# Optimization experiments

Hardware: AMD Instinct MI355X
Metric: run time of the kernel (lower is better)

The kernel has to match this reference:

```python
import jax, jax.numpy as jnp
import numpy as np

BATCH, D_INNER, DT_RANK, N = 256, 5120, 160, 16

def _softplus_thresh(z, threshold=20.0):
    # softplus(z) with beta=1; linear above threshold (matches ttnn.softplus(parameter1=1, parameter2=20))
    return jnp.where(z > threshold, z, jax.nn.softplus(z))

def setup_inputs() -> dict:
    key = jax.random.key(0)
    ks = jax.random.split(key, 9)
    s = lambda d: 1.0 / np.sqrt(d)
    return {
        "x": jax.random.normal(ks[0], (1, 1, BATCH, D_INNER), jnp.float32),
        "h": jax.random.normal(ks[1], (BATCH, D_INNER, N), jnp.float32) * 0.1,
        "W_delta": jax.random.normal(ks[2], (D_INNER, DT_RANK), jnp.float32) * s(D_INNER),
        "W_dt": jax.random.normal(ks[3], (DT_RANK, D_INNER), jnp.float32) * s(DT_RANK),
        "b_dt": jax.random.normal(ks[4], (D_INNER,), jnp.float32) * 0.1,
        "A_log": jax.random.uniform(ks[5], (D_INNER, N), jnp.float32, 0.0, 1.5),
        "W_B": jax.random.normal(ks[6], (D_INNER, N), jnp.float32) * s(D_INNER),
        "W_C": jax.random.normal(ks[7], (D_INNER, N), jnp.float32) * s(D_INNER),
        "D": jax.random.normal(ks[8], (D_INNER,), jnp.float32),
    }

def reference(x, h, W_delta, W_dt, b_dt, A_log, W_B, W_C, D):
    # x: (1,1,B,d_inner) single decode step; h: (B,d_inner,n) SSM state
    xb = x.reshape(BATCH, D_INNER)                           # (B, d)
    # delta = softplus(x @ W_delta @ W_dt + b_dt)           -> (B, d)
    dt = _softplus_thresh((xb @ W_delta) @ W_dt + b_dt)
    A = -jnp.exp(A_log)                                      # (d, n)
    abar = jnp.exp(dt[:, :, None] * A[None, :, :])           # (B, d, n)
    Bp = xb @ W_B                                            # (B, n)
    # bbar * x: delta * B * x, broadcast over state dim
    bx = (dt * xb)[:, :, None] * Bp[:, None, :]              # (B, d, n)
    h_new = abar * h + bx                                    # (B, d, n) new hidden state
    C = xb @ W_C                                             # (B, n)
    y = jnp.einsum("bdn,bn->bd", h_new, C) + xb * D          # readout + skip (D)
    return y.reshape(1, 1, BATCH, D_INNER)
```

## Files before the change

kernel.cpp:

```cpp
#include <hip/hip_runtime.h>
#include <math.h>

#define BATCH 256
#define DIN   5120
#define RANK  160
#define NS    16
#define NCAT  192
#define NSPLIT 40

__global__ __launch_bounds__(256) void k1a_gemm(
    const float* __restrict__ x, const float* __restrict__ Wd,
    const float* __restrict__ WB, const float* __restrict__ WC,
    float* __restrict__ psum)
{
    __shared__ float xT[32][64];
    __shared__ float Wt[32][64];
    const int t  = threadIdx.x;
    const int m0 = blockIdx.x * 64;
    const int n0 = blockIdx.y * 64;
    const int z  = blockIdx.z;
    const int k0 = z * 128;
    const int tm = (t >> 4) * 4;
    const int tn = (t & 15) * 4;

    const int lm  = t >> 2;
    const int lk  = (t & 3) * 8;
    const int ln  = t & 63;
    const int lkb = (t >> 6) * 8;

    const float* wsrc; int wstr;
    {
        const int c = n0 + ln;
        if (c < RANK)            { wsrc = Wd + c;                wstr = RANK; }
        else if (c < RANK + NS)  { wsrc = WB + (c - RANK);       wstr = NS;   }
        else                     { wsrc = WC + (c - RANK - NS);  wstr = NS;   }
    }

    float acc[4][4] = {{0.f}};

    for (int ks = 0; ks < 4; ++ks) {
        const int kb = k0 + ks * 32;
        {
            const float* src = x + (size_t)(m0 + lm) * DIN + kb + lk;
            const float4 a0 = *(const float4*)src;
            const float4 a1 = *(const float4*)(src + 4);
            xT[lk+0][lm]=a0.x; xT[lk+1][lm]=a0.y; xT[lk+2][lm]=a0.z; xT[lk+3][lm]=a0.w;
            xT[lk+4][lm]=a1.x; xT[lk+5][lm]=a1.y; xT[lk+6][lm]=a1.z; xT[lk+7][lm]=a1.w;
        }
        {
            const float* wp = wsrc + (size_t)(kb + lkb) * wstr;
            #pragma unroll
            for (int i = 0; i < 8; ++i) { Wt[lkb + i][ln] = *wp; wp += wstr; }
        }
        __syncthreads();
        #pragma unroll
        for (int k = 0; k < 32; ++k) {
            const float4 a = *(const float4*)&xT[k][tm];
            const float4 b = *(const float4*)&Wt[k][tn];
            acc[0][0] += a.x*b.x; acc[0][1] += a.x*b.y; acc[0][2] += a.x*b.z; acc[0][3] += a.x*b.w;
            acc[1][0] += a.y*b.x; acc[1][1] += a.y*b.y; acc[1][2] += a.y*b.z; acc[1][3] += a.y*b.w;
            acc[2][0] += a.z*b.x; acc[2][1] += a.z*b.y; acc[2][2] += a.z*b.z; acc[2][3] += a.z*b.w;
            acc[3][0] += a.w*b.x; acc[3][1] += a.w*b.y; acc[3][2] += a.w*b.z; acc[3][3] += a.w*b.w;
        }
        __syncthreads();
    }

    float* dst = psum + (size_t)z * (BATCH * NCAT);
    #pragma unroll
    for (int i = 0; i < 4; ++i) {
        const int gm = m0 + tm + i;
        float4 o; o.x = acc[i][0]; o.y = acc[i][1]; o.z = acc[i][2]; o.w = acc[i][3];
        *(float4*)&dst[(size_t)gm * NCAT + n0 + tn] = o;
    }
}

__global__ __launch_bounds__(256) void k1r_reduce(
    const float* __restrict__ psum, float* __restrict__ P,
    float* __restrict__ Bp, float* __restrict__ Cc)
{
    const int o = blockIdx.x * 256 + threadIdx.x;
    float s = 0.f;
    #pragma unroll 8
    for (int z = 0; z < NSPLIT; ++z) s += psum[(size_t)z * (BATCH * NCAT) + o];
    const int gm = o / NCAT;
    const int gc = o - gm * NCAT;
    if (gc < RANK)           P [gm * RANK + gc]             = s;
    else if (gc < RANK + NS) Bp[gm * NS   + gc - RANK]      = s;
    else                     Cc[gm * NS   + gc - RANK - NS] = s;
}

__device__ __forceinline__ float softplus20(float z)
{
    if (z > 20.f) return z;
    return fmaxf(z, 0.f) + log1pf(__expf(-fabsf(z)));
}

__global__ __launch_bounds__(256) void k2a_gemm(
    const float* __restrict__ P, const float* __restrict__ Wdt,
    const float* __restrict__ bdt, float* __restrict__ dtb)
{
    __shared__ float aT[32][64];
    __shared__ float Bt[32][64];
    const int t  = threadIdx.x;
    const int m0 = blockIdx.x * 64;
    const int n0 = blockIdx.y * 64;
    const int tm = (t >> 4) * 4;
    const int tn = (t & 15) * 4;

    const int lm  = t >> 2;
    const int lk  = (t & 3) * 8;
    const int ln  = t & 63;
    const int lkb = (t >> 6) * 8;

    float acc[4][4] = {{0.f}};

    for (int ks = 0; ks < 5; ++ks) {
        const int kb = ks * 32;
        {
            const float* src = P + (size_t)(m0 + lm) * RANK + kb + lk;
            const float4 a0 = *(const float4*)src;
            const float4 a1 = *(const float4*)(src + 4);
            aT[lk+0][lm]=a0.x; aT[lk+1][lm]=a0.y; aT[lk+2][lm]=a0.z; aT[lk+3][lm]=a0.w;
            aT[lk+4][lm]=a1.x; aT[lk+5][lm]=a1.y; aT[lk+6][lm]=a1.z; aT[lk+7][lm]=a1.w;
        }
        {
            const float* wp = Wdt + (size_t)(kb + lkb) * DIN + n0 + ln;
            #pragma unroll
            for (int i = 0; i < 8; ++i) { Bt[lkb + i][ln] = wp[(size_t)i * DIN]; }
        }
        __syncthreads();
        #pragma unroll
        for (int k = 0; k < 32; ++k) {
            const float4 a = *(const float4*)&aT[k][tm];
            const float4 b = *(const float4*)&Bt[k][tn];
            acc[0][0] += a.x*b.x; acc[0][1] += a.x*b.y; acc[0][2] += a.x*b.z; acc[0][3] += a.x*b.w;
            acc[1][0] += a.y*b.x; acc[1][1] += a.y*b.y; acc[1][2] += a.y*b.z; acc[1][3] += a.y*b.w;
            acc[2][0] += a.z*b.x; acc[2][1] += a.z*b.y; acc[2][2] += a.z*b.z; acc[2][3] += a.z*b.w;
            acc[3][0] += a.w*b.x; acc[3][1] += a.w*b.y; acc[3][2] += a.w*b.z; acc[3][3] += a.w*b.w;
        }
        __syncthreads();
    }

    const float4 bz = *(const float4*)&bdt[n0 + tn];
    #pragma unroll
    for (int i = 0; i < 4; ++i) {
        const int gm = m0 + tm + i;
        float4 o;
        o.x = softplus20(acc[i][0] + bz.x);
        o.y = softplus20(acc[i][1] + bz.y);
        o.z = softplus20(acc[i][2] + bz.z);
        o.w = softplus20(acc[i][3] + bz.w);
        *(float4*)&dtb[(size_t)gm * DIN + n0 + tn] = o;
    }
}

__global__ __launch_bounds__(256) void k3_ssm(
    const float* __restrict__ dtb, const float* __restrict__ x,
    const float* __restrict__ h, const float* __restrict__ A_log,
    const float* __restrict__ Bp, const float* __restrict__ Cc,
    const float* __restrict__ Dv, float* __restrict__ y)
{
    const int t    = threadIdx.x;
    const int lane = t & 63;
    const int wv   = t >> 6;
    const int b    = blockIdx.x / 20;
    const int d0   = (blockIdx.x % 20) * 256 + wv * 64;

    const int v = lane & 3;
    const int j = lane >> 2;

    const float4 B4 = *(const float4*)(Bp + b * NS + v * 4);
    const float4 C4 = *(const float4*)(Cc + b * NS + v * 4);

    float res[4];
    #pragma unroll
    for (int q = 0; q < 4; ++q) {
        const int c = d0 + q * 16 + j;
        const float dtv = dtb[(size_t)b * DIN + c];
        const float xv  = x  [(size_t)b * DIN + c];
        const float dtx = dtv * xv;
        const float4 h4 = *(const float4*)(h     + ((size_t)b * DIN + c) * NS + v * 4);
        const float4 a4 = *(const float4*)(A_log + (size_t)c * NS + v * 4);
        float s;
        s  = (exp2f(dtv * (-1.442695041f * __expf(a4.x))) * h4.x + dtx * B4.x) * C4.x;
        s += (exp2f(dtv * (-1.442695041f * __expf(a4.y))) * h4.y + dtx * B4.y) * C4.y;
        s += (exp2f(dtv * (-1.442695041f * __expf(a4.z))) * h4.z + dtx * B4.z) * C4.z;
        s += (exp2f(dtv * (-1.442695041f * __expf(a4.w))) * h4.w + dtx * B4.w) * C4.w;
        if (v == 0) s += xv * Dv[c];
        res[q] = s;
    }

    #pragma unroll
    for (int q = 0; q < 4; ++q) {
        res[q] += __shfl_xor(res[q], 1, 64);
        res[q] += __shfl_xor(res[q], 2, 64);
    }
    if (v == 0) {
        #pragma unroll
        for (int q = 0; q < 4; ++q)
            y[(size_t)b * DIN + d0 + q * 16 + j] = res[q];
    }
}

extern "C" void kernel_launch(void* const* d_in, const int* in_sizes, int n_in,
                              void* d_out, int out_size, void* d_ws, size_t ws_size,
                              hipStream_t stream)
{
    const float* x     = (const float*)d_in[0];
    const float* h     = (const float*)d_in[1];
    const float* Wd    = (const float*)d_in[2];
    const float* Wdt   = (const float*)d_in[3];
    const float* bdt   = (const float*)d_in[4];
    const float* A_log = (const float*)d_in[5];
    const float* WB    = (const float*)d_in[6];
    const float* WC    = (const float*)d_in[7];
    const float* Dv    = (const float*)d_in[8];
    float* out = (float*)d_out;

    float* psum = (float*)d_ws;
    float* P    = psum + (size_t)NSPLIT * BATCH * NCAT;
    float* Bp   = P  + BATCH * RANK;
    float* Cc   = Bp + BATCH * NS;
    float* dtb  = Cc + BATCH * NS;

    k1a_gemm  <<<dim3(4, 3, NSPLIT), 256, 0, stream>>>(x, Wd, WB, WC, psum);
    k1r_reduce<<<dim3(NCAT),         256, 0, stream>>>(psum, P, Bp, Cc);
    k2a_gemm  <<<dim3(4, 80),        256, 0, stream>>>(P, Wdt, bdt, dtb);
    k3_ssm    <<<dim3(BATCH * 20),   256, 0, stream>>>(dtb, x, h, A_log, Bp, Cc, Dv, out);
}
```

Measured before the change: 182.2 us.

## Fuse dt GEMM into SSM kernel and precompute scaled A in reduce

Merges the second projection GEMM (P @ W_dt + softplus) into the SSM update kernel. Each block computes dt for 8 batch rows by 256 channels into shared memory and then consumes it directly, which removes the dtb round trip through global memory and one launch. The reduce kernel now also precomputes -log2(e)*exp(A_log) once, so the SSM loop no longer does a per-element exp on A. The fused GEMM is a plain per-thread dot product that reads the W_dt column uncoalesced-strided over k and P through broadcast loads, with no shared-memory tiling, so it may cost more ALU and memory time than the old tiled GEMM.

```diff
diff --git a/kernel.cpp b/kernel.cpp
--- a/kernel.cpp
+++ b/kernel.cpp
@@ -7,6 +7,7 @@
 #define NS    16
 #define NCAT  192
 #define NSPLIT 40
+#define BQ    8
 
 __global__ __launch_bounds__(256) void k1a_gemm(
     const float* __restrict__ x, const float* __restrict__ Wd,
@@ -75,18 +76,24 @@
 }
 
 __global__ __launch_bounds__(256) void k1r_reduce(
-    const float* __restrict__ psum, float* __restrict__ P,
-    float* __restrict__ Bp, float* __restrict__ Cc)
-{
-    const int o = blockIdx.x * 256 + threadIdx.x;
-    float s = 0.f;
-    #pragma unroll 8
-    for (int z = 0; z < NSPLIT; ++z) s += psum[(size_t)z * (BATCH * NCAT) + o];
-    const int gm = o / NCAT;
-    const int gc = o - gm * NCAT;
-    if (gc < RANK)           P [gm * RANK + gc]             = s;
-    else if (gc < RANK + NS) Bp[gm * NS   + gc - RANK]      = s;
-    else                     Cc[gm * NS   + gc - RANK - NS] = s;
+    const float* __restrict__ psum, const float* __restrict__ A_log,
+    float* __restrict__ P, float* __restrict__ Bp, float* __restrict__ Cc,
+    float* __restrict__ A2t)
+{
+    const int g = blockIdx.x * 256 + threadIdx.x;
+    A2t[g] = -1.442695041f * __expf(A_log[g]);
+
+    if (blockIdx.x < NCAT) {
+        const int o = blockIdx.x * 256 + threadIdx.x;
+        float s = 0.f;
+        #pragma unroll 8
+        for (int z = 0; z < NSPLIT; ++z) s += psum[(size_t)z * (BATCH * NCAT) + o];
+        const int gm = o / NCAT;
+        const int gc = o - gm * NCAT;
+        if (gc < RANK)           P [gm * RANK + gc]             = s;
+        else if (gc < RANK + NS) Bp[gm * NS   + gc - RANK]      = s;
+        else                     Cc[gm * NS   + gc - RANK - NS] = s;
+    }
 }
 
 __device__ __forceinline__ float softplus20(float z)
@@ -95,110 +102,82 @@
     return fmaxf(z, 0.f) + log1pf(__expf(-fabsf(z)));
 }
 
-__global__ __launch_bounds__(256) void k2a_gemm(
+__global__ __launch_bounds__(256) void k23_ssm(
     const float* __restrict__ P, const float* __restrict__ Wdt,
-    const float* __restrict__ bdt, float* __restrict__ dtb)
-{
-    __shared__ float aT[32][64];
-    __shared__ float Bt[32][64];
-    const int t  = threadIdx.x;
-    const int m0 = blockIdx.x * 64;
-    const int n0 = blockIdx.y * 64;
-    const int tm = (t >> 4) * 4;
-    const int tn = (t & 15) * 4;
-
-    const int lm  = t >> 2;
-    const int lk  = (t & 3) * 8;
-    const int ln  = t & 63;
-    const int lkb = (t >> 6) * 8;
-
-    float acc[4][4] = {{0.f}};
-
-    for (int ks = 0; ks < 5; ++ks) {
-        const int kb = ks * 32;
-        {
-            const float* src = P + (size_t)(m0 + lm) * RANK + kb + lk;
-            const float4 a0 = *(const float4*)src;
-            const float4 a1 = *(const float4*)(src + 4);
-            aT[lk+0][lm]=a0.x; aT[lk+1][lm]=a0.y; aT[lk+2][lm]=a0.z; aT[lk+3][lm]=a0.w;
-            aT[lk+4][lm]=a1.x; aT[lk+5][lm]=a1.y; aT[lk+6][lm]=a1.z; aT[lk+7][lm]=a1.w;
-        }
-        {
-            const float* wp = Wdt + (size_t)(kb + lkb) * DIN + n0 + ln;
-            #pragma unroll
-            for (int i = 0; i < 8; ++i) { Bt[lkb + i][ln] = wp[(size_t)i * DIN]; }
-        }
-        __syncthreads();
-        #pragma unroll
-        for (int k = 0; k < 32; ++k) {
-            const float4 a = *(const float4*)&aT[k][tm];
-            const float4 b = *(const float4*)&Bt[k][tn];
-            acc[0][0] += a.x*b.x; acc[0][1] += a.x*b.y; acc[0][2] += a.x*b.z; acc[0][3] += a.x*b.w;
-            acc[1][0] += a.y*b.x; acc[1][1] += a.y*b.y; acc[1][2] += a.y*b.z; acc[1][3] += a.y*b.w;
-            acc[2][0] += a.z*b.x; acc[2][1] += a.z*b.y; acc[2][2] += a.z*b.z; acc[2][3] += a.z*b.w;
-            acc[3][0] += a.w*b.x; acc[3][1] += a.w*b.y; acc[3][2] += a.w*b.z; acc[3][3] += a.w*b.w;
-        }
-        __syncthreads();
-    }
-
-    const float4 bz = *(const float4*)&bdt[n0 + tn];
-    #pragma unroll
-    for (int i = 0; i < 4; ++i) {
-        const int gm = m0 + tm + i;
-        float4 o;
-        o.x = softplus20(acc[i][0] + bz.x);
-        o.y = softplus20(acc[i][1] + bz.y);
-        o.z = softplus20(acc[i][2] + bz.z);
-        o.w = softplus20(acc[i][3] + bz.w);
-        *(float4*)&dtb[(size_t)gm * DIN + n0 + tn] = o;
-    }
-}
-
-__global__ __launch_bounds__(256) void k3_ssm(
-    const float* __restrict__ dtb, const float* __restrict__ x,
-    const float* __restrict__ h, const float* __restrict__ A_log,
+    const float* __restrict__ bdt, const float* __restrict__ x,
+    const float* __restrict__ h, const float* __restrict__ A2t,
     const float* __restrict__ Bp, const float* __restrict__ Cc,
     const float* __restrict__ Dv, float* __restrict__ y)
 {
-    const int t    = threadIdx.x;
+    __shared__ float sdt[BQ][256];
+
+    const int t  = threadIdx.x;
+    const int ct = blockIdx.x % 20;
+    const int bg = blockIdx.x / 20;
+    const int c0 = ct * 256;
+    const int b0 = bg * BQ;
+
+    {
+        const int c = c0 + t;
+        float acc[BQ];
+        #pragma unroll
+        for (int b = 0; b < BQ; ++b) acc[b] = 0.f;
+        const float* wcol = Wdt + c;
+        const float* Pb   = P + (size_t)b0 * RANK;
+        #pragma unroll 4
+        for (int k = 0; k < RANK; ++k) {
+            const float w = wcol[(size_t)k * DIN];
+            #pragma unroll
+            for (int b = 0; b < BQ; ++b) acc[b] += Pb[b * RANK + k] * w;
+        }
+        const float bb = bdt[c];
+        #pragma unroll
+        for (int b = 0; b < BQ; ++b) sdt[b][t] = softplus20(acc[b] + bb);
+    }
+    __syncthreads();
+
     const int lane = t & 63;
     const int wv   = t >> 6;
-    const int b    = blockIdx.x / 20;
-    const int d0   = (blockIdx.x % 20) * 256 + wv * 64;
-
-    const int v = lane & 3;
-    const int j = lane >> 2;
-
-    const float4 B4 = *(const float4*)(Bp + b * NS + v * 4);
-    const float4 C4 = *(const float4*)(Cc + b * NS + v * 4);
-
-    float res[4];
+    const int v    = lane & 3;
+    const int j    = lane >> 2;
+    const int cb   = c0 + wv * 64;
+
+    float4 A2q[4];
     #pragma unroll
-    for (int q = 0; q < 4; ++q) {
-        const int c = d0 + q * 16 + j;
-        const float dtv = dtb[(size_t)b * DIN + c];
-        const float xv  = x  [(size_t)b * DIN + c];
-        const float dtx = dtv * xv;
-        const float4 h4 = *(const float4*)(h     + ((size_t)b * DIN + c) * NS + v * 4);
-        const float4 a4 = *(const float4*)(A_log + (size_t)c * NS + v * 4);
-        float s;
-        s  = (exp2f(dtv * (-1.442695041f * __expf(a4.x))) * h4.x + dtx * B4.x) * C4.x;
-        s += (exp2f(dtv * (-1.442695041f * __expf(a4.y))) * h4.y + dtx * B4.y) * C4.y;
-        s += (exp2f(dtv * (-1.442695041f * __expf(a4.z))) * h4.z + dtx * B4.z) * C4.z;
-        s += (exp2f(dtv * (-1.442695041f * __expf(a4.w))) * h4.w + dtx * B4.w) * C4.w;
-        if (v == 0) s += xv * Dv[c];
-        res[q] = s;
-    }
-
-    #pragma unroll
-    for (int q = 0; q < 4; ++q) {
-        res[q] += __shfl_xor(res[q], 1, 64);
-        res[q] += __shfl_xor(res[q], 2, 64);
-    }
-    if (v == 0) {
-        #pragma unroll
-        for (int q = 0; q < 4; ++q)
-            y[(size_t)b * DIN + d0 + q * 16 + j] = res[q];
+    for (int q = 0; q < 4; ++q)
+        A2q[q] = *(const float4*)(A2t + (size_t)(cb + q * 16 + j) * NS + v * 4);
+
+    #pragma unroll 2
+    for (int b = 0; b < BQ; ++b) {
+        const int gb = b0 + b;
+        const float4 B4 = *(const float4*)(Bp + gb * NS + v * 4);
+        const float4 C4 = *(const float4*)(Cc + gb * NS + v * 4);
+        float res[4];
+        #pragma unroll
+        for (int q = 0; q < 4; ++q) {
+            const int cq  = cb + q * 16 + j;
+            const float dtv = sdt[b][wv * 64 + q * 16 + j];
+            const float xv  = x[(size_t)gb * DIN + cq];
+            const float dtx = dtv * xv;
+            const float4 h4 = *(const float4*)(h + ((size_t)gb * DIN + cq) * NS + v * 4);
+            float s;
+            s  = (exp2f(dtv * A2q[q].x) * h4.x + dtx * B4.x) * C4.x;
+            s += (exp2f(dtv * A2q[q].y) * h4.y + dtx * B4.y) * C4.y;
+            s += (exp2f(dtv * A2q[q].z) * h4.z + dtx * B4.z) * C4.z;
+            s += (exp2f(dtv * A2q[q].w) * h4.w + dtx * B4.w) * C4.w;
+            if (v == 0) s += xv * Dv[cq];
+            res[q] = s;
+        }
+        #pragma unroll
+        for (int q = 0; q < 4; ++q) {
+            res[q] += __shfl_xor(res[q], 1, 64);
+            res[q] += __shfl_xor(res[q], 2, 64);
+        }
+        if (v == 0) {
+            #pragma unroll
+            for (int q = 0; q < 4; ++q)
+                y[(size_t)gb * DIN + cb + q * 16 + j] = res[q];
+        }
     }
 }
 
@@ -221,10 +200,9 @@
     float* P    = psum + (size_t)NSPLIT * BATCH * NCAT;
     float* Bp   = P  + BATCH * RANK;
     float* Cc   = Bp + BATCH * NS;
-    float* dtb  = Cc + BATCH * NS;
-
-    k1a_gemm  <<<dim3(4, 3, NSPLIT), 256, 0, stream>>>(x, Wd, WB, WC, psum);
-    k1r_reduce<<<dim3(NCAT),         256, 0, stream>>>(psum, P, Bp, Cc);
-    k2a_gemm  <<<dim3(4, 80),        256, 0, stream>>>(P, Wdt, bdt, dtb);
-    k3_ssm    <<<dim3(BATCH * 20),   256, 0, stream>>>(dtb, x, h, A_log, Bp, Cc, Dv, out);
-}
+    float* A2t  = Cc + BATCH * NS;
+
+    k1a_gemm  <<<dim3(4, 3, NSPLIT),   256, 0, stream>>>(x, Wd, WB, WC, psum);
+    k1r_reduce<<<dim3(320),            256, 0, stream>>>(psum, A_log, P, Bp, Cc, A2t);
+    k23_ssm   <<<dim3(20 * BATCH/BQ),  256, 0, stream>>>(P, Wdt, bdt, x, h, A2t, Bp, Cc, Dv, out);
+}
```

After: 198.1 us. 8.7% more time.

## Fuse dt GEMM with SSM update and precompute scaled A in reduce kernel

Applied to the files above, without the earlier changes.

Merges the dt projection GEMM and the SSM state-update kernel so each block computes a 64x64 tile of softplus(dt) into shared memory and consumes it directly, removing the dtb global round trip and one launch. The reduce kernel is widened to also precompute -log2(e)*exp(A_log) once, so the SSM stage no longer recomputes an exp per element per batch. The fused grid has only 320 blocks each looping over 16 batches per wave, which cuts parallelism for the memory-bound h stream and adds 16KB of shared memory per block.

```diff
diff --git a/kernel.cpp b/kernel.cpp
--- a/kernel.cpp
+++ b/kernel.cpp
@@ -75,18 +75,24 @@
 }
 
 __global__ __launch_bounds__(256) void k1r_reduce(
-    const float* __restrict__ psum, float* __restrict__ P,
-    float* __restrict__ Bp, float* __restrict__ Cc)
-{
-    const int o = blockIdx.x * 256 + threadIdx.x;
-    float s = 0.f;
-    #pragma unroll 8
-    for (int z = 0; z < NSPLIT; ++z) s += psum[(size_t)z * (BATCH * NCAT) + o];
-    const int gm = o / NCAT;
-    const int gc = o - gm * NCAT;
-    if (gc < RANK)           P [gm * RANK + gc]             = s;
-    else if (gc < RANK + NS) Bp[gm * NS   + gc - RANK]      = s;
-    else                     Cc[gm * NS   + gc - RANK - NS] = s;
+    const float* __restrict__ psum, const float* __restrict__ A_log,
+    float* __restrict__ P, float* __restrict__ Bp, float* __restrict__ Cc,
+    float* __restrict__ A2t)
+{
+    const int g = blockIdx.x * 256 + threadIdx.x;
+    A2t[g] = -1.442695041f * __expf(A_log[g]);
+
+    if (blockIdx.x < NCAT) {
+        const int o = blockIdx.x * 256 + threadIdx.x;
+        float s = 0.f;
+        #pragma unroll 8
+        for (int z = 0; z < NSPLIT; ++z) s += psum[(size_t)z * (BATCH * NCAT) + o];
+        const int gm = o / NCAT;
+        const int gc = o - gm * NCAT;
+        if (gc < RANK)           P [gm * RANK + gc]             = s;
+        else if (gc < RANK + NS) Bp[gm * NS   + gc - RANK]      = s;
+        else                     Cc[gm * NS   + gc - RANK - NS] = s;
+    }
 }
 
 __device__ __forceinline__ float softplus20(float z)
@@ -95,110 +101,116 @@
     return fmaxf(z, 0.f) + log1pf(__expf(-fabsf(z)));
 }
 
-__global__ __launch_bounds__(256) void k2a_gemm(
+__global__ __launch_bounds__(256) void k23_ssm(
     const float* __restrict__ P, const float* __restrict__ Wdt,
-    const float* __restrict__ bdt, float* __restrict__ dtb)
+    const float* __restrict__ bdt, const float* __restrict__ x,
+    const float* __restrict__ h, const float* __restrict__ A2t,
+    const float* __restrict__ Bp, const float* __restrict__ Cc,
+    const float* __restrict__ Dv, float* __restrict__ y)
 {
     __shared__ float aT[32][64];
     __shared__ float Bt[32][64];
+    __shared__ float sdt[64][64];
+
     const int t  = threadIdx.x;
-    const int m0 = blockIdx.x * 64;
-    const int n0 = blockIdx.y * 64;
-    const int tm = (t >> 4) * 4;
-    const int tn = (t & 15) * 4;
-
-    const int lm  = t >> 2;
-    const int lk  = (t & 3) * 8;
-    const int ln  = t & 63;
-    const int lkb = (t >> 6) * 8;
-
-    float acc[4][4] = {{0.f}};
-
-    for (int ks = 0; ks < 5; ++ks) {
-        const int kb = ks * 32;
-        {
-            const float* src = P + (size_t)(m0 + lm) * RANK + kb + lk;
-            const float4 a0 = *(const float4*)src;
-            const float4 a1 = *(const float4*)(src + 4);
-            aT[lk+0][lm]=a0.x; aT[lk+1][lm]=a0.y; aT[lk+2][lm]=a0.z; aT[lk+3][lm]=a0.w;
-            aT[lk+4][lm]=a1.x; aT[lk+5][lm]=a1.y; aT[lk+6][lm]=a1.z; aT[lk+7][lm]=a1.w;
-        }
-        {
-            const float* wp = Wdt + (size_t)(kb + lkb) * DIN + n0 + ln;
+    const int c0 = blockIdx.x * 64;
+    const int b0 = blockIdx.y * 64;
+
+    {
+        const int tm = (t >> 4) * 4;
+        const int tn = (t & 15) * 4;
+        const int lm  = t >> 2;
+        const int lk  = (t & 3) * 8;
+        const int ln  = t & 63;
+        const int lkb = (t >> 6) * 8;
+
+        float acc[4][4] = {{0.f}};
+
+        for (int ks = 0; ks < 5; ++ks) {
+            const int kb = ks * 32;
+            {
+                const float* src = P + (size_t)(b0 + lm) * RANK + kb + lk;
+                const float4 a0 = *(const float4*)src;
+                const float4 a1 = *(const float4*)(src + 4);
+                aT[lk+0][lm]=a0.x; aT[lk+1][lm]=a0.y; aT[lk+2][lm]=a0.z; aT[lk+3][lm]=a0.w;
+                aT[lk+4][lm]=a1.x; aT[lk+5][lm]=a1.y; aT[lk+6][lm]=a1.z; aT[lk+7][lm]=a1.w;
+            }
+            {
+                const float* wp = Wdt + (size_t)(kb + lkb) * DIN + c0 + ln;
+                #pragma unroll
+                for (int i = 0; i < 8; ++i) { Bt[lkb + i][ln] = wp[(size_t)i * DIN]; }
+            }
+            __syncthreads();
             #pragma unroll
-            for (int i = 0; i < 8; ++i) { Bt[lkb + i][ln] = wp[(size_t)i * DIN]; }
-        }
-        __syncthreads();
-        #pragma unroll
-        for (int k = 0; k < 32; ++k) {
-            const float4 a = *(const float4*)&aT[k][tm];
-            const float4 b = *(const float4*)&Bt[k][tn];
-            acc[0][0] += a.x*b.x; acc[0][1] += a.x*b.y; acc[0][2] += a.x*b.z; acc[0][3] += a.x*b.w;
-            acc[1][0] += a.y*b.x; acc[1][1] += a.y*b.y; acc[1][2] += a.y*b.z; acc[1][3] += a.y*b.w;
-            acc[2][0] += a.z*b.x; acc[2][1] += a.z*b.y; acc[2][2] += a.z*b.z; acc[2][3] += a.z*b.w;
-            acc[3][0] += a.w*b.x; acc[3][1] += a.w*b.y; acc[3][2] += a.w*b.z; acc[3][3] += a.w*b.w;
-        }
-        __syncthreads();
-    }
-
-    const float4 bz = *(const float4*)&bdt[n0 + tn];
-    #pragma unroll
-    for (int i = 0; i < 4; ++i) {
-        const int gm = m0 + tm + i;
-        float4 o;
-        o.x = softplus20(acc[i][0] + bz.x);
-        o.y = softplus20(acc[i][1] + bz.y);
-        o.z = softplus20(acc[i][2] + bz.z);
-        o.w = softplus20(acc[i][3] + bz.w);
-        *(float4*)&dtb[(size_t)gm * DIN + n0 + tn] = o;
-    }
-}
-
-__global__ __launch_bounds__(256) void k3_ssm(
-    const float* __restrict__ dtb, const float* __restrict__ x,
-    const float* __restrict__ h, const float* __restrict__ A_log,
-    const float* __restrict__ Bp, const float* __restrict__ Cc,
-    const float* __restrict__ Dv, float* __restrict__ y)
-{
-    const int t    = threadIdx.x;
+            for (int k = 0; k < 32; ++k) {
+                const float4 a = *(const float4*)&aT[k][tm];
+                const float4 b = *(const float4*)&Bt[k][tn];
+                acc[0][0] += a.x*b.x; acc[0][1] += a.x*b.y; acc[0][2] += a.x*b.z; acc[0][3] += a.x*b.w;
+                acc[1][0] += a.y*b.x; acc[1][1] += a.y*b.y; acc[1][2] += a.y*b.z; acc[1][3] += a.y*b.w;
+                acc[2][0] += a.z*b.x; acc[2][1] += a.z*b.y; acc[2][2] += a.z*b.z; acc[2][3] += a.z*b.w;
+                acc[3][0] += a.w*b.x; acc[3][1] += a.w*b.y; acc[3][2] += a.w*b.z; acc[3][3] += a.w*b.w;
+            }
+            __syncthreads();
+        }
+
+        const float4 bz = *(const float4*)&bdt[c0 + tn];
+        #pragma unroll
+        for (int i = 0; i < 4; ++i) {
+            float4 o;
+            o.x = softplus20(acc[i][0] + bz.x);
+            o.y = softplus20(acc[i][1] + bz.y);
+            o.z = softplus20(acc[i][2] + bz.z);
+            o.w = softplus20(acc[i][3] + bz.w);
+            *(float4*)&sdt[tm + i][tn] = o;
+        }
+    }
+    __syncthreads();
+
     const int lane = t & 63;
     const int wv   = t >> 6;
-    const int b    = blockIdx.x / 20;
-    const int d0   = (blockIdx.x % 20) * 256 + wv * 64;
-
-    const int v = lane & 3;
-    const int j = lane >> 2;
-
-    const float4 B4 = *(const float4*)(Bp + b * NS + v * 4);
-    const float4 C4 = *(const float4*)(Cc + b * NS + v * 4);
-
-    float res[4];
+    const int v    = lane & 3;
+    const int j    = lane >> 2;
+
+    float4 A2q[4]; float dvq[4];
     #pragma unroll
     for (int q = 0; q < 4; ++q) {
-        const int c = d0 + q * 16 + j;
-        const float dtv = dtb[(size_t)b * DIN + c];
-        const float xv  = x  [(size_t)b * DIN + c];
-        const float dtx = dtv * xv;
-        const float4 h4 = *(const float4*)(h     + ((size_t)b * DIN + c) * NS + v * 4);
-        const float4 a4 = *(const float4*)(A_log + (size_t)c * NS + v * 4);
-        float s;
-        s  = (exp2f(dtv * (-1.442695041f * __expf(a4.x))) * h4.x + dtx * B4.x) * C4.x;
-        s += (exp2f(dtv * (-1.442695041f * __expf(a4.y))) * h4.y + dtx * B4.y) * C4.y;
-        s += (exp2f(dtv * (-1.442695041f * __expf(a4.z))) * h4.z + dtx * B4.z) * C4.z;
-        s += (exp2f(dtv * (-1.442695041f * __expf(a4.w))) * h4.w + dtx * B4.w) * C4.w;
-        if (v == 0) s += xv * Dv[c];
-        res[q] = s;
-    }
-
-    #pragma unroll
-    for (int q = 0; q < 4; ++q) {
-        res[q] += __shfl_xor(res[q], 1, 64);
-        res[q] += __shfl_xor(res[q], 2, 64);
-    }
-    if (v == 0) {
-        #pragma unroll
-        for (int q = 0; q < 4; ++q)
-            y[(size_t)b * DIN + d0 + q * 16 + j] = res[q];
+        const int c = c0 + q * 16 + j;
+        A2q[q] = *(const float4*)(A2t + (size_t)c * NS + v * 4);
+        dvq[q] = Dv[c];
+    }
+
+    #pragma unroll 4
+    for (int bi = 0; bi < 16; ++bi) {
+        const int bl = wv * 16 + bi;
+        const int gb = b0 + bl;
+        const float4 B4 = *(const float4*)(Bp + gb * NS + v * 4);
+        const float4 C4 = *(const float4*)(Cc + gb * NS + v * 4);
+        float res[4];
+        #pragma unroll
+        for (int q = 0; q < 4; ++q) {
+            const int c = c0 + q * 16 + j;
+            const float dtv = sdt[bl][q * 16 + j];
+            const float xv  = x[(size_t)gb * DIN + c];
+            const float dtx = dtv * xv;
+            const float4 h4 = *(const float4*)(h + ((size_t)gb * DIN + c) * NS + v * 4);
+            float s;
+            s  = (exp2f(dtv * A2q[q].x) * h4.x + dtx * B4.x) * C4.x;
+            s += (exp2f(dtv * A2q[q].y) * h4.y + dtx * B4.y) * C4.y;
+            s += (exp2f(dtv * A2q[q].z) * h4.z + dtx * B4.z) * C4.z;
+            s += (exp2f(dtv * A2q[q].w) * h4.w + dtx * B4.w) * C4.w;
+            if (v == 0) s += xv * dvq[q];
+            res[q] = s;
+        }
+        #pragma unroll
+        for (int q = 0; q < 4; ++q) {
+            res[q] += __shfl_xor(res[q], 1, 64);
+            res[q] += __shfl_xor(res[q], 2, 64);
+        }
+        if (v == 0) {
+            #pragma unroll
+            for (int q = 0; q < 4; ++q)
+                y[(size_t)gb * DIN + c0 + q * 16 + j] = res[q];
+        }
     }
 }
 
@@ -221,10 +233,9 @@
     float* P    = psum + (size_t)NSPLIT * BATCH * NCAT;
     float* Bp   = P  + BATCH * RANK;
     float* Cc   = Bp + BATCH * NS;
-    float* dtb  = Cc + BATCH * NS;
+    float* A2t  = Cc + BATCH * NS;
 
     k1a_gemm  <<<dim3(4, 3, NSPLIT), 256, 0, stream>>>(x, Wd, WB, WC, psum);
-    k1r_reduce<<<dim3(NCAT),         256, 0, stream>>>(psum, P, Bp, Cc);
-    k2a_gemm  <<<dim3(4, 80),        256, 0, stream>>>(P, Wdt, bdt, dtb);
-    k3_ssm    <<<dim3(BATCH * 20),   256, 0, stream>>>(dtb, x, h, A_log, Bp, Cc, Dv, out);
-}
+    k1r_reduce<<<dim3(320),          256, 0, stream>>>(psum, A_log, P, Bp, Cc, A2t);
+    k23_ssm   <<<dim3(80, 4),        256, 0, stream>>>(P, Wdt, bdt, x, h, A2t, Bp, Cc, Dv, out);
+}
```

Result: no change. 181.9 us (-0.2%).
